# Performance work log

Measured on AMD Instinct MI355X. Metric: run time of the kernel, lower is better.

The kernel has to match this reference:

```python
import jax, jax.numpy as jnp
import numpy as np
from jax import lax

C = 384  # in_planes


def setup_inputs() -> dict:
    key = jax.random.key(0)
    k1, k2 = jax.random.split(key)
    x = jax.random.normal(k1, (16, C, 128, 128), dtype=jnp.float32)
    k = jax.random.normal(k2, (C, 1, 3, 3), dtype=jnp.float32)  # (in_planes, 1, kh, kw)
    return {"x": x, "k": k}


def reference(x, k):
    # Depthwise conv: equivalent to the original per-channel F.conv2d loop + concat,
    # fused into a single grouped conv with feature_group_count = C.
    return lax.conv_general_dilated(
        x, k,
        window_strides=(1, 1),
        padding=((1, 1), (1, 1)),
        rhs_dilation=(1, 1),
        dimension_numbers=("NCHW", "OIHW", "NCHW"),
        feature_group_count=C,
    )
```

## Files before the change

kernel.cpp:

```cpp
#include <hip/hip_runtime.h>


#define CC 384
#define HH 128
#define WW 128
#define NN 16

__global__ __launch_bounds__(256) void dwconv3x3(const float* __restrict__ x,
                                                 const float* __restrict__ k,
                                                 float* __restrict__ out) {
    const int b    = blockIdx.x;
    const int half = b & 1;
    const int nc   = b >> 1;
    const int c    = nc % CC;

    const int strip = half * 256 + (int)threadIdx.x;
    const int w0 = (strip & 31) << 2;
    const int h0 = (strip >> 5) << 3;

    const float* xp = x   + (size_t)nc * (HH * WW);
    float*       op = out + (size_t)nc * (HH * WW);

    const float* kp = k + c * 9;
    const float w00 = kp[0], w01 = kp[1], w02 = kp[2];
    const float w10 = kp[3], w11 = kp[4], w12 = kp[5];
    const float w20 = kp[6], w21 = kp[7], w22 = kp[8];

    float r[10][6];

    #pragma unroll
    for (int t = 0; t < 10; ++t) {
        const int h = h0 - 1 + t;
        if (h < 0 || h >= HH) {
            #pragma unroll
            for (int j = 0; j < 6; ++j) r[t][j] = 0.f;
        } else {
            const float* p = xp + h * WW + w0;
            const float4 m = *reinterpret_cast<const float4*>(p);
            r[t][1] = m.x; r[t][2] = m.y; r[t][3] = m.z; r[t][4] = m.w;
            r[t][0] = (w0 > 0)      ? p[-1] : 0.f;
            r[t][5] = (w0 + 4 < WW) ? p[4]  : 0.f;
        }
    }

    #pragma unroll
    for (int i = 0; i < 8; ++i) {
        float o[4];
        #pragma unroll
        for (int j = 0; j < 4; ++j) {
            o[j] = r[i][j]     * w00 + r[i][j + 1]     * w01 + r[i][j + 2]     * w02
                 + r[i + 1][j] * w10 + r[i + 1][j + 1] * w11 + r[i + 1][j + 2] * w12
                 + r[i + 2][j] * w20 + r[i + 2][j + 1] * w21 + r[i + 2][j + 2] * w22;
        }
        *reinterpret_cast<float4*>(op + (h0 + i) * WW + w0) =
            make_float4(o[0], o[1], o[2], o[3]);
    }
}

extern "C" void kernel_launch(void* const* d_in, const int* in_sizes, int n_in,
                              void* d_out, int out_size, void* d_ws, size_t ws_size,
                              hipStream_t stream) {
    const float* x = (const float*)d_in[0];
    const float* k = (const float*)d_in[1];
    float*     out = (float*)d_out;

    const int blocks = NN * CC * 2;
    dwconv3x3<<<blocks, 256, 0, stream>>>(x, k, out);
}
```

Baseline: 171.9 us.

## Use rolling row window with shuffle-based halo and taller per-thread strips

Each thread now computes 16 output rows using a 3-row rolling register window instead of loading a 10-row buffer for 8 rows. Horizontal halo values are obtained via wave shuffles instead of extra scalar global loads. The grid is halved to one block per channel-image. This reduces redundant global loads and register use but serializes loads with compute within each thread, which may lower memory-level parallelism.

```diff
diff --git a/kernel.cpp b/kernel.cpp
--- a/kernel.cpp
+++ b/kernel.cpp
@@ -9,14 +9,13 @@
 __global__ __launch_bounds__(256) void dwconv3x3(const float* __restrict__ x,
                                                  const float* __restrict__ k,
                                                  float* __restrict__ out) {
-    const int b    = blockIdx.x;
-    const int half = b & 1;
-    const int nc   = b >> 1;
-    const int c    = nc % CC;
+    const int nc = blockIdx.x;
+    const int c  = nc % CC;
 
-    const int strip = half * 256 + (int)threadIdx.x;
-    const int w0 = (strip & 31) << 2;
-    const int h0 = (strip >> 5) << 3;
+    const int tid   = (int)threadIdx.x;
+    const int w_idx = tid & 31;
+    const int w0    = w_idx << 2;
+    const int h0    = (tid >> 5) << 4;
 
     const float* xp = x   + (size_t)nc * (HH * WW);
     float*       op = out + (size_t)nc * (HH * WW);
@@ -26,35 +25,45 @@
     const float w10 = kp[3], w11 = kp[4], w12 = kp[5];
     const float w20 = kp[6], w21 = kp[7], w22 = kp[8];
 
-    float r[10][6];
+    const bool lEdge = (w_idx == 0);
+    const bool rEdge = (w_idx == 31);
+
+    float r[3][6];
+
+#define LOAD_ROW(h, ri)                                                        \
+    {                                                                          \
+        float4 m = make_float4(0.f, 0.f, 0.f, 0.f);                            \
+        if ((unsigned)(h) < (unsigned)HH)                                      \
+            m = *reinterpret_cast<const float4*>(xp + (h) * WW + w0);          \
+        r[ri][1] = m.x; r[ri][2] = m.y; r[ri][3] = m.z; r[ri][4] = m.w;        \
+        const float lv = __shfl_up(m.w, 1);                                    \
+        const float rv = __shfl_down(m.x, 1);                                  \
+        r[ri][0] = lEdge ? 0.f : lv;                                           \
+        r[ri][5] = rEdge ? 0.f : rv;                                           \
+    }
+
+    LOAD_ROW(h0 - 1, 0)
+    LOAD_ROW(h0,     1)
 
     #pragma unroll
-    for (int t = 0; t < 10; ++t) {
-        const int h = h0 - 1 + t;
-        if (h < 0 || h >= HH) {
-            #pragma unroll
-            for (int j = 0; j < 6; ++j) r[t][j] = 0.f;
-        } else {
-            const float* p = xp + h * WW + w0;
-            const float4 m = *reinterpret_cast<const float4*>(p);
-            r[t][1] = m.x; r[t][2] = m.y; r[t][3] = m.z; r[t][4] = m.w;
-            r[t][0] = (w0 > 0)      ? p[-1] : 0.f;
-            r[t][5] = (w0 + 4 < WW) ? p[4]  : 0.f;
-        }
-    }
+    for (int i = 0; i < 16; ++i) {
+        const int h = h0 + i;
+        LOAD_ROW(h + 1, (i + 2) % 3)
 
-    #pragma unroll
-    for (int i = 0; i < 8; ++i) {
         float o[4];
         #pragma unroll
         for (int j = 0; j < 4; ++j) {
-            o[j] = r[i][j]     * w00 + r[i][j + 1]     * w01 + r[i][j + 2]     * w02
-                 + r[i + 1][j] * w10 + r[i + 1][j + 1] * w11 + r[i + 1][j + 2] * w12
-                 + r[i + 2][j] * w20 + r[i + 2][j + 1] * w21 + r[i + 2][j + 2] * w22;
+            o[j] = r[i % 3][j]           * w00 + r[i % 3][j + 1]       * w01
+                 + r[i % 3][j + 2]       * w02
+                 + r[(i + 1) % 3][j]     * w10 + r[(i + 1) % 3][j + 1] * w11
+                 + r[(i + 1) % 3][j + 2] * w12
+                 + r[(i + 2) % 3][j]     * w20 + r[(i + 2) % 3][j + 1] * w21
+                 + r[(i + 2) % 3][j + 2] * w22;
         }
-        *reinterpret_cast<float4*>(op + (h0 + i) * WW + w0) =
+        *reinterpret_cast<float4*>(op + h * WW + w0) =
             make_float4(o[0], o[1], o[2], o[3]);
     }
+#undef LOAD_ROW
 }
 
 extern "C" void kernel_launch(void* const* d_in, const int* in_sizes, int n_in,
@@ -64,6 +73,6 @@
     const float* k = (const float*)d_in[1];
     float*     out = (float*)d_out;
 
-    const int blocks = NN * CC * 2;
+    const int blocks = NN * CC;
     dwconv3x3<<<blocks, 256, 0, stream>>>(x, k, out);
 }
```

New measurement: 164.0 us. 4.6% less time.
